# Kernel optimization log

Hardware: AMD Instinct MI355X
Metric: run time of the kernel (lower is better)

The kernel has to match this reference:

```python
import jax, jax.numpy as jnp
import numpy as np

T_LEN, BATCH, IN_SIZE, HID = 512, 64, 1024, 1024
EPS = 1e-6


def layer_norm(x, alpha, beta, eps=EPS):
    # Matches torch: mean over last dim, UNBIASED variance (ddof=1)
    mu = jnp.mean(x, axis=-1, keepdims=True)
    var = jnp.var(x, axis=-1, keepdims=True, ddof=1)
    xn = (x - mu) / jnp.sqrt(var + eps)
    return alpha * xn + beta


def setup_inputs() -> dict:
    key = jax.random.key(0)
    ks = jax.random.split(key, 12)
    std = 1.0 / np.sqrt(HID)
    u = lambda k, shape: jax.random.uniform(k, shape, jnp.float32, -std, std)
    return {
        "x": jax.random.normal(ks[0], (T_LEN, BATCH, IN_SIZE), jnp.float32),
        "Wi": u(ks[1], (4 * HID, IN_SIZE)),
        "bi": u(ks[2], (4 * HID,)),
        "Wh": u(ks[3], (4 * HID, HID)),
        "bh": u(ks[4], (4 * HID,)),
        "g_i2h": u(ks[5], (4 * HID,)),
        "b_i2h": u(ks[6], (4 * HID,)),
        "g_h2h": u(ks[7], (4 * HID,)),
        "b_h2h": u(ks[8], (4 * HID,)),
        "g_cell": u(ks[9], (HID,)),
        "b_cell": u(ks[10], (HID,)),
    }


def reference(x, Wi, bi, Wh, bh, g_i2h, b_i2h, g_h2h, b_h2h, g_cell, b_cell):
    # Faithful to the source: h and c are NEVER updated inside the loop
    # (the original code omits h = h_t / c = c_t), so every timestep sees
    # the initial zero state -> fully parallel over time.
    T, B, _ = x.shape
    H = Wh.shape[1]
    h0 = jnp.zeros((B, H), x.dtype)
    c0 = jnp.zeros((B, H), x.dtype)

    i2h = layer_norm(jnp.einsum('tbi,gi->tbg', x, Wi) + bi, g_i2h, b_i2h)  # [T,B,4H]
    h2h = layer_norm(h0 @ Wh.T + bh, g_h2h, b_h2h)                          # [B,4H]
    preact = i2h + h2h                                                      # [T,B,4H]

    gates = jax.nn.sigmoid(preact[..., :3 * H])
    g_t = jnp.tanh(preact[..., 3 * H:])
    f_t = gates[..., H:2 * H]
    o_t = gates[..., 2 * H:3 * H]
    # i_t = gates[..., :H] is computed in the original but unused

    c_t = c0 * f_t + (1.0 - f_t) * g_t
    c_t = layer_norm(c_t, g_cell, b_cell)
    h_t = o_t * jnp.tanh(c_t)  # [T,B,H]

    return h_t, h_t[-1]
```

## Files before the change

kernel.cpp:

```cpp
#include <hip/hip_runtime.h>
#include <hip/hip_bf16.h>
#include <stdint.h>


#define MROWS 32768L
#define NCOLS 4096
#define KDIM  1024

typedef __bf16 bf16x8 __attribute__((ext_vector_type(8)));
typedef __bf16 bf16x4 __attribute__((ext_vector_type(4)));
typedef float  f32x4  __attribute__((ext_vector_type(4)));

__device__ float g_Cvec[4096];

__device__ __forceinline__ void gload16(char* lds, const char* g) {
  __builtin_amdgcn_global_load_lds(
      (const __attribute__((address_space(1))) char*)g,
      (__attribute__((address_space(3))) char*)lds, 16, 0, 0);
}

__device__ __forceinline__ void block_reduce2(float& a, float& b, float* red, int tid) {
#pragma unroll
  for (int m = 32; m > 0; m >>= 1) {
    a += __shfl_xor(a, m, 64);
    b += __shfl_xor(b, m, 64);
  }
  const int lane = tid & 63, wid = tid >> 6;
  if (lane == 0) { red[wid] = a; red[4 + wid] = b; }
  __syncthreads();
  a = red[0] + red[1] + red[2] + red[3];
  b = red[4] + red[5] + red[6] + red[7];
  __syncthreads();
}

__global__ __launch_bounds__(256) void cast_kernel(const float4* __restrict__ in,
                                                   bf16x4* __restrict__ out, int n4) {
  int i = blockIdx.x * 256 + threadIdx.x;
  const int stride = gridDim.x * 256;
  for (; i < n4; i += stride) {
    const float4 v = in[i];
    bf16x4 o = { (__bf16)v.x, (__bf16)v.y, (__bf16)v.z, (__bf16)v.w };
    out[i] = o;
  }
}

__global__ __launch_bounds__(256) void prep_kernel(const float* __restrict__ bh,
                                                   const float* __restrict__ b_i2h,
                                                   const float* __restrict__ g_h2h,
                                                   const float* __restrict__ b_h2h) {
  __shared__ float red[8];
  const int tid = threadIdx.x;
  float v[16];
  float s = 0.f, ss = 0.f;
#pragma unroll
  for (int u = 0; u < 16; ++u) {
    v[u] = bh[tid + u * 256];
    s += v[u]; ss += v[u] * v[u];
  }
  block_reduce2(s, ss, red, tid);
  const float mu  = s * (1.f / 4096.f);
  const float var = (ss - 4096.f * mu * mu) * (1.f / 4095.f);
  const float rs  = rsqrtf(var + 1e-6f);
#pragma unroll
  for (int u = 0; u < 16; ++u) {
    const int g = tid + u * 256;
    g_Cvec[g] = b_i2h[g] + g_h2h[g] * ((v[u] - mu) * rs) + b_h2h[g];
  }
}


#define PH_MID() do { asm volatile("" ::: "memory"); __builtin_amdgcn_s_barrier(); \
    asm volatile("s_waitcnt lgkmcnt(0)" ::: "memory"); \
    __builtin_amdgcn_sched_barrier(0); __builtin_amdgcn_s_setprio(1); } while (0)

#define PH_END() do { __builtin_amdgcn_s_setprio(0); \
    asm volatile("" ::: "memory"); __builtin_amdgcn_s_barrier(); } while (0)

#define STG_A(s, h) { char* d_ = Al + (((s) & 1) << 15) + ((h) << 14); \
    const char* g_ = Ag + (long)(h) * 262144 + (s) * 128; \
    gload16(d_, g_); gload16(d_ + 8192, g_ + 131072); }

#define STG_B(s, h) { char* d_ = Bl + (((s) & 1) << 15) + ((h) << 14); \
    const char* g_ = Bg + (long)(h) * 262144 + (s) * 128; \
    gload16(d_, g_); gload16(d_ + 8192, g_ + 131072); }

#define RD_A(arr, c) { _Pragma("unroll") for (int mi_ = 0; mi_ < 4; ++mi_) { \
    const char* p_ = Ahalf + (((c) * 64 + mi_ * 16 + fr) << 7); \
    arr[mi_][0] = *(const bf16x8*)(p_ + cb0); \
    arr[mi_][1] = *(const bf16x8*)(p_ + cb1); } }

#define RD_B(g) { _Pragma("unroll") for (int nj_ = 0; nj_ < 2; ++nj_) { \
    const char* p_ = Bhalf + ((brow0 + (g) * 32 + nj_ * 16 + fr) << 7); \
    b[nj_][0] = *(const bf16x8*)(p_ + cb0); \
    b[nj_][1] = *(const bf16x8*)(p_ + cb1); } }

#define MM_Q(arr, c, g) { _Pragma("unroll") for (int mi_ = 0; mi_ < 4; ++mi_) { \
    _Pragma("unroll") for (int nj_ = 0; nj_ < 2; ++nj_) { \
      acc[(c)*4+mi_][(g)*2+nj_] = __builtin_amdgcn_mfma_f32_16x16x32_bf16( \
          arr[mi_][0], b[nj_][0], acc[(c)*4+mi_][(g)*2+nj_], 0, 0, 0); \
      acc[(c)*4+mi_][(g)*2+nj_] = __builtin_amdgcn_mfma_f32_16x16x32_bf16( \
          arr[mi_][1], b[nj_][1], acc[(c)*4+mi_][(g)*2+nj_], 0, 0, 0); } } }

__global__ __launch_bounds__(512, 2) void gemm_kernel(const __bf16* __restrict__ A,
                                                      const __bf16* __restrict__ B,
                                                      __bf16* __restrict__ Y, long r0) {
  __shared__ __align__(16) __bf16 As[2 * 2 * 8192];
  __shared__ __align__(16) __bf16 Bs[2 * 2 * 8192];

  const int tid  = threadIdx.x;
  const int lane = tid & 63;
  const int wid  = tid >> 6;
  const int wr   = wid >> 2;
  const int wc   = wid & 3;

  const int nwg = gridDim.x;
  const int q8 = nwg >> 3, r8 = nwg & 7;
  const int xcd = blockIdx.x & 7, rest = blockIdx.x >> 3;
  const int wgid = (xcd < r8 ? xcd * (q8 + 1) : r8 * (q8 + 1) + (xcd - r8) * q8) + rest;
  const long m0 = (long)(wgid >> 4) * 256;
  const long n0 = (long)(wgid & 15) * 256;

  const int scol = (((tid & 7) ^ ((tid >> 3) & 7)) << 4);
  const char* Ag = (const char*)(A + (r0 + m0) * KDIM) + (long)(tid >> 3) * 2048 + scol;
  const char* Bg = (const char*)(B + n0 * KDIM) + (long)(tid >> 3) * 2048 + scol;
  char* Al = (char*)As + tid * 16;
  char* Bl = (char*)Bs + tid * 16;

  const int fr  = lane & 15;
  const int sw  = (fr & 7) << 4;
  const int cb0 = (((lane >> 4) << 4)) ^ sw;
  const int cb1 = (64 | ((lane >> 4) << 4)) ^ sw;
  const int brow0 = (wc & 1) << 6;

  f32x4 acc[8][4];
  const f32x4 z = {0.f, 0.f, 0.f, 0.f};
#pragma unroll
  for (int i = 0; i < 8; ++i)
#pragma unroll
    for (int j = 0; j < 4; ++j) acc[i][j] = z;

  STG_A(0, 0); STG_A(0, 1); STG_B(0, 0); STG_B(0, 1); STG_A(1, 0); STG_A(1, 1);
  asm volatile("s_waitcnt vmcnt(4)" ::: "memory");
  __builtin_amdgcn_s_barrier();

  bf16x8 aa[4][2], ab[4][2], b[2][2];

#pragma unroll 2
  for (int t = 0; t < 16; ++t) {
    const char* Ahalf = (const char*)As + ((t & 1) << 15) + (wr << 14);
    const char* Bhalf = (const char*)Bs + ((t & 1) << 15) + ((wc >> 1) << 14);

    RD_A(aa, 0); RD_B(0);
    if (t + 1 < 16) STG_B(t + 1, 0);
    PH_MID(); MM_Q(aa, 0, 0); PH_END();
    RD_A(ab, 1);
    if (t + 1 < 16) STG_B(t + 1, 1);
    PH_MID(); MM_Q(ab, 1, 0); PH_END();
    RD_B(1);
    if (t + 2 < 16) STG_A(t + 2, 0);
    PH_MID(); MM_Q(ab, 1, 1); PH_END();
    if (t + 2 < 16) STG_A(t + 2, 1);
    PH_MID(); MM_Q(aa, 0, 1);
    __builtin_amdgcn_s_setprio(0);
    if (t == 14)      { asm volatile("s_waitcnt vmcnt(0)" ::: "memory"); }
    else if (t < 14)  { asm volatile("s_waitcnt vmcnt(4)" ::: "memory"); }
    asm volatile("" ::: "memory");
    __builtin_amdgcn_s_barrier();
  }

  const long mrow = m0 + wr * 128 + ((lane >> 4) << 2);
  const long ncol = n0 + wc * 64 + fr;
  __bf16* Yp = Y + mrow * NCOLS + ncol;
#pragma unroll
  for (int c = 0; c < 2; ++c)
#pragma unroll
    for (int mi = 0; mi < 4; ++mi)
#pragma unroll
      for (int nj = 0; nj < 4; ++nj)
#pragma unroll
        for (int r = 0; r < 4; ++r)
          Yp[(long)(c * 64 + mi * 16 + r) * NCOLS + nj * 16] = (__bf16)acc[c * 4 + mi][nj][r];
}

__global__ __launch_bounds__(256) void pass2_kernel(const __bf16* __restrict__ Yw,
                                                    const float* __restrict__ bi,
                                                    const float* __restrict__ g_i2h,
                                                    const float* __restrict__ g_cell,
                                                    const float* __restrict__ b_cell,
                                                    float* __restrict__ out, long r0) {
  __shared__ float p0[4096];
  __shared__ float red[8];
  const int tid  = threadIdx.x;
  const long row = r0 + blockIdx.x;
  const bf16x8* yv = (const bf16x8*)(Yw + (long)blockIdx.x * NCOLS);

  float s = 0.f, ss = 0.f;
#pragma unroll
  for (int it = 0; it < 2; ++it) {
    const int ch = tid + it * 256;
    const bf16x8 v = yv[ch];
    const float4 b0 = ((const float4*)bi)[ch * 2];
    const float4 b1 = ((const float4*)bi)[ch * 2 + 1];
    float p[8];
    p[0] = (float)v[0] + b0.x;  p[1] = (float)v[1] + b0.y;
    p[2] = (float)v[2] + b0.z;  p[3] = (float)v[3] + b0.w;
    p[4] = (float)v[4] + b1.x;  p[5] = (float)v[5] + b1.y;
    p[6] = (float)v[6] + b1.z;  p[7] = (float)v[7] + b1.w;
#pragma unroll
    for (int u = 0; u < 8; ++u) {
      p0[ch * 8 + u] = p[u];
      s += p[u];
      ss += p[u] * p[u];
    }
  }
  block_reduce2(s, ss, red, tid);
  const float mu  = s * (1.f / 4096.f);
  const float var = (ss - 4096.f * mu * mu) * (1.f / 4095.f);
  const float rs  = rsqrtf(var + 1e-6f);

  float cc[4], oo[4];
  float s2 = 0.f, ss2 = 0.f;
#pragma unroll
  for (int u = 0; u < 4; ++u) {
    const int j = tid + u * 256;
    const float pf = g_i2h[1024 + j] * ((p0[1024 + j] - mu) * rs) + g_Cvec[1024 + j];
    const float po = g_i2h[2048 + j] * ((p0[2048 + j] - mu) * rs) + g_Cvec[2048 + j];
    const float pg = g_i2h[3072 + j] * ((p0[3072 + j] - mu) * rs) + g_Cvec[3072 + j];
    const float f  = 1.f / (1.f + __expf(-pf));
    oo[u] = 1.f / (1.f + __expf(-po));
    const float e2 = __expf(2.f * pg);
    const float gt = (e2 - 1.f) / (e2 + 1.f);
    cc[u] = (1.f - f) * gt;
    s2 += cc[u]; ss2 += cc[u] * cc[u];
  }
  block_reduce2(s2, ss2, red, tid);
  const float mu2  = s2 * (1.f / 1024.f);
  const float var2 = (ss2 - 1024.f * mu2 * mu2) * (1.f / 1023.f);
  const float rs2  = rsqrtf(var2 + 1e-6f);

  const long obase = row * 1024;
#pragma unroll
  for (int u = 0; u < 4; ++u) {
    const int j = tid + u * 256;
    const float cn = g_cell[j] * ((cc[u] - mu2) * rs2) + b_cell[j];
    const float e2 = __expf(2.f * cn);
    const float th = (e2 - 1.f) / (e2 + 1.f);
    const float h  = oo[u] * th;
    out[obase + j] = h;
    if (row >= MROWS - 64)
      out[MROWS * 1024 + ((row - (MROWS - 64)) << 10) + j] = h;
  }
}

extern "C" void kernel_launch(void* const* d_in, const int* in_sizes, int n_in,
                              void* d_out, int out_size, void* d_ws, size_t ws_size,
                              hipStream_t stream) {
  (void)in_sizes; (void)n_in; (void)out_size;
  const float* x      = (const float*)d_in[0];
  const float* Wi     = (const float*)d_in[1];
  const float* bi     = (const float*)d_in[2];
  const float* bh     = (const float*)d_in[4];
  const float* g_i2h  = (const float*)d_in[5];
  const float* b_i2h  = (const float*)d_in[6];
  const float* g_h2h  = (const float*)d_in[7];
  const float* b_h2h  = (const float*)d_in[8];
  const float* g_cell = (const float*)d_in[9];
  const float* b_cell = (const float*)d_in[10];
  float* out = (float*)d_out;

  __bf16* xb = (__bf16*)d_out;
  __bf16* wb = (__bf16*)((char*)d_out + 67108864);
  __bf16* y  = (__bf16*)d_ws;

  cast_kernel<<<2048, 256, 0, stream>>>((const float4*)x, (bf16x4*)xb, 33554432 / 4);
  cast_kernel<<<1024, 256, 0, stream>>>((const float4*)Wi, (bf16x4*)wb, 4194304 / 4);
  prep_kernel<<<1, 256, 0, stream>>>(bh, b_i2h, g_h2h, b_h2h);

  long max_rows = (long)(ws_size / (NCOLS * 2)) & ~255L;
  if (max_rows > MROWS) max_rows = MROWS;
  if (max_rows < 256)   max_rows = 256;
  for (long rbase = 0; rbase < MROWS; rbase += max_rows) {
    const long rows = (MROWS - rbase < max_rows) ? (MROWS - rbase) : max_rows;
    gemm_kernel<<<dim3((rows / 256) * 16), 512, 0, stream>>>(xb, wb, y, rbase);
    pass2_kernel<<<dim3(rows), 256, 0, stream>>>(y, bi, g_i2h, g_cell, b_cell, out, rbase);
  }
}
```

Measured before the change: 486.8 us.

## Software-pipeline LDS fragment reads across tiles and chunk GEMM into smaller row blocks

The GEMM main loop is reorganised so the next tile's A/B fragments are read from LDS during the current tile's last MFMA quadrant. It uses double-buffered register fragments, issues staging loads earlier, and has fewer barriers per phase. The bf16 casts of x and Wi move from the output buffer into the workspace. The GEMM/pass2 loop is capped at 8192 rows per chunk, likely so the intermediate stays cache-resident between the GEMM and the epilogue. The cost is more launches and higher register pressure from the extra fragment buffers.

```diff
diff --git a/kernel.cpp b/kernel.cpp
--- a/kernel.cpp
+++ b/kernel.cpp
@@ -69,12 +69,11 @@
 }
 
 
-#define PH_MID() do { asm volatile("" ::: "memory"); __builtin_amdgcn_s_barrier(); \
-    asm volatile("s_waitcnt lgkmcnt(0)" ::: "memory"); \
-    __builtin_amdgcn_sched_barrier(0); __builtin_amdgcn_s_setprio(1); } while (0)
-
-#define PH_END() do { __builtin_amdgcn_s_setprio(0); \
-    asm volatile("" ::: "memory"); __builtin_amdgcn_s_barrier(); } while (0)
+#define LGKM0() do { asm volatile("s_waitcnt lgkmcnt(0)" ::: "memory"); \
+    __builtin_amdgcn_sched_barrier(0); } while (0)
+#define BAR()   do { asm volatile("" ::: "memory"); __builtin_amdgcn_s_barrier(); \
+    asm volatile("" ::: "memory"); } while (0)
+#define VMCNT(n) asm volatile("s_waitcnt vmcnt(" #n ")" ::: "memory")
 
 #define STG_A(s, h) { char* d_ = Al + (((s) & 1) << 15) + ((h) << 14); \
     const char* g_ = Ag + (long)(h) * 262144 + (s) * 128; \
@@ -84,22 +83,42 @@
     const char* g_ = Bg + (long)(h) * 262144 + (s) * 128; \
     gload16(d_, g_); gload16(d_ + 8192, g_ + 131072); }
 
-#define RD_A(arr, c) { _Pragma("unroll") for (int mi_ = 0; mi_ < 4; ++mi_) { \
-    const char* p_ = Ahalf + (((c) * 64 + mi_ * 16 + fr) << 7); \
+#define ABASE(t) ((const char*)As + (((t) & 1) << 15) + (wr << 14))
+#define BBASE(t) ((const char*)Bs + (((t) & 1) << 15) + ((wc >> 1) << 14))
+
+#define RD_Ax(arr, Ahalf, c) { _Pragma("unroll") for (int mi_ = 0; mi_ < 4; ++mi_) { \
+    const char* p_ = (Ahalf) + (((c) * 64 + mi_ * 16 + fr) << 7); \
     arr[mi_][0] = *(const bf16x8*)(p_ + cb0); \
     arr[mi_][1] = *(const bf16x8*)(p_ + cb1); } }
 
-#define RD_B(g) { _Pragma("unroll") for (int nj_ = 0; nj_ < 2; ++nj_) { \
-    const char* p_ = Bhalf + ((brow0 + (g) * 32 + nj_ * 16 + fr) << 7); \
-    b[nj_][0] = *(const bf16x8*)(p_ + cb0); \
-    b[nj_][1] = *(const bf16x8*)(p_ + cb1); } }
-
-#define MM_Q(arr, c, g) { _Pragma("unroll") for (int mi_ = 0; mi_ < 4; ++mi_) { \
+#define RD_Bx(arr, Bhalf, g) { _Pragma("unroll") for (int nj_ = 0; nj_ < 2; ++nj_) { \
+    const char* p_ = (Bhalf) + ((brow0 + (g) * 32 + nj_ * 16 + fr) << 7); \
+    arr[nj_][0] = *(const bf16x8*)(p_ + cb0); \
+    arr[nj_][1] = *(const bf16x8*)(p_ + cb1); } }
+
+#define MMQ(X, Y, c, g) { _Pragma("unroll") for (int mi_ = 0; mi_ < 4; ++mi_) { \
     _Pragma("unroll") for (int nj_ = 0; nj_ < 2; ++nj_) { \
       acc[(c)*4+mi_][(g)*2+nj_] = __builtin_amdgcn_mfma_f32_16x16x32_bf16( \
-          arr[mi_][0], b[nj_][0], acc[(c)*4+mi_][(g)*2+nj_], 0, 0, 0); \
+          X[mi_][0], Y[nj_][0], acc[(c)*4+mi_][(g)*2+nj_], 0, 0, 0); \
       acc[(c)*4+mi_][(g)*2+nj_] = __builtin_amdgcn_mfma_f32_16x16x32_bf16( \
-          arr[mi_][1], b[nj_][1], acc[(c)*4+mi_][(g)*2+nj_], 0, 0, 0); } } }
+          X[mi_][1], Y[nj_][1], acc[(c)*4+mi_][(g)*2+nj_], 0, 0, 0); } } }
+
+#define SETP1() __builtin_amdgcn_s_setprio(1)
+#define SETP0() __builtin_amdgcn_s_setprio(0)
+
+#define TILE(t, Ac, An, Bc, Bn, G1, G2) { \
+    const char* AhC = ABASE(t); const char* BhC = BBASE(t); \
+    const char* AhN = ABASE((t) + 1); const char* BhN = BBASE((t) + 1); \
+     LGKM0(); RD_Ax(An, AhC, 1); if (G1) STG_B((t) + 1, 1); \
+    SETP1(); MMQ(Ac, Bc, 0, 0); SETP0(); BAR(); \
+     LGKM0(); RD_Bx(Bn, BhC, 1); \
+    SETP1(); MMQ(An, Bc, 1, 0); SETP0(); BAR(); \
+     LGKM0(); if (G2) STG_A((t) + 2, 0); \
+    SETP1(); MMQ(An, Bn, 1, 1); SETP0(); \
+    if (G2) { VMCNT(2); } else { VMCNT(0); } BAR(); \
+     if (G1) { RD_Ax(An, AhN, 0); RD_Bx(Bc, BhN, 0); } \
+    if (G2) { STG_A((t) + 2, 1); STG_B((t) + 2, 0); } \
+    SETP1(); MMQ(Ac, Bn, 0, 1); SETP0(); BAR(); }
 
 __global__ __launch_bounds__(512, 2) void gemm_kernel(const __bf16* __restrict__ A,
                                                       const __bf16* __restrict__ B,
@@ -139,34 +158,22 @@
 #pragma unroll
     for (int j = 0; j < 4; ++j) acc[i][j] = z;
 
-  STG_A(0, 0); STG_A(0, 1); STG_B(0, 0); STG_B(0, 1); STG_A(1, 0); STG_A(1, 1);
-  asm volatile("s_waitcnt vmcnt(4)" ::: "memory");
-  __builtin_amdgcn_s_barrier();
-
-  bf16x8 aa[4][2], ab[4][2], b[2][2];
-
-#pragma unroll 2
-  for (int t = 0; t < 16; ++t) {
-    const char* Ahalf = (const char*)As + ((t & 1) << 15) + (wr << 14);
-    const char* Bhalf = (const char*)Bs + ((t & 1) << 15) + ((wc >> 1) << 14);
-
-    RD_A(aa, 0); RD_B(0);
-    if (t + 1 < 16) STG_B(t + 1, 0);
-    PH_MID(); MM_Q(aa, 0, 0); PH_END();
-    RD_A(ab, 1);
-    if (t + 1 < 16) STG_B(t + 1, 1);
-    PH_MID(); MM_Q(ab, 1, 0); PH_END();
-    RD_B(1);
-    if (t + 2 < 16) STG_A(t + 2, 0);
-    PH_MID(); MM_Q(ab, 1, 1); PH_END();
-    if (t + 2 < 16) STG_A(t + 2, 1);
-    PH_MID(); MM_Q(aa, 0, 1);
-    __builtin_amdgcn_s_setprio(0);
-    if (t == 14)      { asm volatile("s_waitcnt vmcnt(0)" ::: "memory"); }
-    else if (t < 14)  { asm volatile("s_waitcnt vmcnt(4)" ::: "memory"); }
-    asm volatile("" ::: "memory");
-    __builtin_amdgcn_s_barrier();
-  }
+  bf16x8 A0[4][2], A1[4][2], B0[2][2], B1[2][2];
+
+  STG_A(0, 0); STG_A(0, 1); STG_B(0, 0); STG_B(0, 1);
+  STG_A(1, 0); STG_A(1, 1); STG_B(1, 0);
+  VMCNT(6);
+  BAR();
+  RD_Ax(A0, ABASE(0), 0); RD_Bx(B0, BBASE(0), 0);
+
+#pragma unroll 1
+  for (int tt = 0; tt < 7; ++tt) {
+    const int t = tt * 2;
+    TILE(t,     A0, A1, B0, B1, true, true);
+    TILE(t + 1, A1, A0, B0, B1, true, true);
+  }
+  TILE(14, A0, A1, B0, B1, true,  false);
+  TILE(15, A1, A0, B0, B1, false, false);
 
   const long mrow = m0 + wr * 128 + ((lane >> 4) << 2);
   const long ncol = n0 + wc * 64 + fr;
@@ -268,17 +275,18 @@
   const float* b_cell = (const float*)d_in[10];
   float* out = (float*)d_out;
 
-  __bf16* xb = (__bf16*)d_out;
-  __bf16* wb = (__bf16*)((char*)d_out + 67108864);
-  __bf16* y  = (__bf16*)d_ws;
+  __bf16* xb = (__bf16*)d_ws;
+  __bf16* wb = (__bf16*)((char*)d_ws + 67108864);
+  __bf16* y  = (__bf16*)((char*)d_ws + 75497472);
 
   cast_kernel<<<2048, 256, 0, stream>>>((const float4*)x, (bf16x4*)xb, 33554432 / 4);
   cast_kernel<<<1024, 256, 0, stream>>>((const float4*)Wi, (bf16x4*)wb, 4194304 / 4);
   prep_kernel<<<1, 256, 0, stream>>>(bh, b_i2h, g_h2h, b_h2h);
 
-  long max_rows = (long)(ws_size / (NCOLS * 2)) & ~255L;
-  if (max_rows > MROWS) max_rows = MROWS;
-  if (max_rows < 256)   max_rows = 256;
+  long avail = (long)ws_size - 75497472L;
+  long max_rows = (avail / (NCOLS * 2)) & ~255L;
+  if (max_rows > 8192) max_rows = 8192;
+  if (max_rows < 256)  max_rows = 256;
   for (long rbase = 0; rbase < MROWS; rbase += max_rows) {
     const long rows = (MROWS - rbase < max_rows) ? (MROWS - rbase) : max_rows;
     gemm_kernel<<<dim3((rows / 256) * 16), 512, 0, stream>>>(xb, wb, y, rbase);
```

Result: faster. 431.9 us (-11.3%).
